# Kernel optimization log

Measured on AMD Instinct MI355X. Metric: run time of the kernel, lower is better.

Reference implementation:

```python
import jax, jax.numpy as jnp
import numpy as np

S = 2048          # sequence length (single prefill sequence)
HID = 4096        # hidden_size
NH, NKV, HD = 32, 8, 128   # q heads, kv heads, head_dim
THETA = 10000.0
SCALE = HD ** -0.5


def setup_inputs() -> dict:
    key = jax.random.key(0)
    k1, k2, k3 = jax.random.split(key, 3)
    hidden_states = jax.random.normal(k1, (S, HID), jnp.float32)
    positions = jnp.arange(S, dtype=jnp.int32)
    W_qkv = jax.random.normal(k2, (HID, (NH + 2 * NKV) * HD), jnp.float32) * 0.02
    W_o = jax.random.normal(k3, (NH * HD, HID), jnp.float32) * 0.02
    return {"hidden_states": hidden_states, "positions": positions,
            "W_qkv": W_qkv, "W_o": W_o}


def _rope(x, positions):
    # x: [T, H, HD]; neox-style RoPE (rotate halves, is_neox_style=True)
    half = HD // 2
    inv_freq = 1.0 / (THETA ** (jnp.arange(half, dtype=jnp.float32) / half))
    freqs = positions.astype(jnp.float32)[:, None] * inv_freq[None, :]  # [T, half]
    cos = jnp.cos(freqs)[:, None, :]
    sin = jnp.sin(freqs)[:, None, :]
    x1, x2 = x[..., :half], x[..., half:]
    return jnp.concatenate([x1 * cos - x2 * sin, x2 * cos + x1 * sin], axis=-1)


def reference(hidden_states, positions, W_qkv, W_o):
    # fused QKV projection then split (q_size = NH*HD, kv_size = NKV*HD)
    qkv = hidden_states @ W_qkv                      # [S, (NH+2*NKV)*HD]
    q, k, v = jnp.split(qkv, [NH * HD, NH * HD + NKV * HD], axis=1)
    q = _rope(q.reshape(S, NH, HD), positions)       # [S, NH, HD]
    k = _rope(k.reshape(S, NKV, HD), positions)      # [S, NKV, HD]
    v = v.reshape(S, NKV, HD)
    # GQA: broadcast kv heads to query heads
    rep = NH // NKV
    k = jnp.repeat(k, rep, axis=1)                   # [S, NH, HD]
    v = jnp.repeat(v, rep, axis=1)
    scores = jnp.einsum('qhd,khd->hqk', q, k) * SCALE  # [NH, S, S]
    causal = jnp.tril(jnp.ones((S, S), dtype=bool))
    scores = jnp.where(causal[None], scores, jnp.finfo(scores.dtype).min)
    attn = jax.nn.softmax(scores, axis=-1)
    out = jnp.einsum('hqk,khd->qhd', attn, v).reshape(S, NH * HD)
    return out @ W_o                                 # [S, HID]
```

## Files before the change

kernel.cpp:

```cpp
#include <hip/hip_runtime.h>
#include <math.h>
#include <stdint.h>

#define S_LEN 2048
#define HID 4096
#define NH 32
#define NKV 8
#define HD 128
#define QKV_N ((NH + 2*NKV) * HD)
#define NQK (NH + NKV)
static __device__ __constant__ const float SCALE_F = 0.08838834764831845f;

typedef __bf16 bf16x8 __attribute__((ext_vector_type(8)));
typedef __bf16 bf16x4 __attribute__((ext_vector_type(4)));
typedef float  f32x4  __attribute__((ext_vector_type(4)));
typedef uint32_t u32x4 __attribute__((ext_vector_type(4)));

#define GLD_LDS(gptr, lptr) \
  __builtin_amdgcn_global_load_lds( \
      (const __attribute__((address_space(1))) uint32_t*)(gptr), \
      (__attribute__((address_space(3))) uint32_t*)(lptr), 16, 0, 0)

__global__ void cast_bf16_kernel(const float4* __restrict__ in, __bf16* __restrict__ out, int n4) {
  int i = blockIdx.x * blockDim.x + threadIdx.x;
  if (i >= n4) return;
  float4 v = in[i];
  bf16x4 o = { (__bf16)v.x, (__bf16)v.y, (__bf16)v.z, (__bf16)v.w };
  *(bf16x4*)(out + (size_t)i * 4) = o;
}

__global__ void transpose_cast_kernel(const float* __restrict__ in, __bf16* __restrict__ out,
                                      int R, int C) {
  __shared__ float tile[32][33];
  int bx = blockIdx.x * 32;
  int by = blockIdx.y * 32;
  int tx = threadIdx.x, ty = threadIdx.y;
  for (int i = 0; i < 32; i += 8)
    tile[ty + i][tx] = in[(size_t)(by + ty + i) * C + bx + tx];
  __syncthreads();
  for (int i = 0; i < 32; i += 8)
    out[(size_t)(bx + ty + i) * R + by + tx] = (__bf16)tile[tx][ty + i];
}

__global__ void transpose_v_kernel(const __bf16* __restrict__ qkv, __bf16* __restrict__ Vt) {
  __shared__ __bf16 tile[32][33];
  int kvh = blockIdx.z;
  int sb = blockIdx.x * 32;
  int db = blockIdx.y * 32;
  int tx = threadIdx.x, ty = threadIdx.y;
  const __bf16* src = qkv + (size_t)(NH + NKV) * HD + (size_t)kvh * HD;
  for (int i = 0; i < 32; i += 8)
    tile[ty + i][tx] = src[(size_t)(sb + ty + i) * QKV_N + db + tx];
  __syncthreads();
  for (int i = 0; i < 32; i += 8)
    Vt[((size_t)kvh * HD + db + ty + i) * S_LEN + sb + tx] = tile[tx][ty + i];
}

__global__ void rope_kernel(const __bf16* __restrict__ qkv, const int* __restrict__ pos,
                            __bf16* __restrict__ Qr, __bf16* __restrict__ Kr) {
  int idx = blockIdx.x * blockDim.x + threadIdx.x;
  int half = idx & 63;
  int t = idx >> 6;
  int hh = t % NQK;
  int s = t / NQK;
  if (s >= S_LEN) return;
  float p = (float)pos[s];
  float inv_freq = exp2f((float)half * -0.2076205059304601f);
  float ang = p * inv_freq;
  float cs = cosf(ang), sn = sinf(ang);
  const __bf16* src; __bf16* dst;
  if (hh < NH) {
    src = qkv + (size_t)s * QKV_N + (size_t)hh * HD;
    dst = Qr + ((size_t)s * NH + hh) * HD;
  } else {
    int kh = hh - NH;
    src = qkv + (size_t)s * QKV_N + (size_t)NH * HD + (size_t)kh * HD;
    dst = Kr + ((size_t)s * NKV + kh) * HD;
  }
  float x1 = (float)src[half], x2 = (float)src[half + 64];
  dst[half]      = (__bf16)(x1 * cs - x2 * sn);
  dst[half + 64] = (__bf16)(x2 * cs + x1 * sn);
}

template <typename OutT>
__global__ __launch_bounds__(512, 2) void gemm8p_kernel(const __bf16* __restrict__ A,
                                                        const __bf16* __restrict__ Bt,
                                                        OutT* __restrict__ C,
                                                        int M, int N, int K) {
  __shared__ __align__(16) __bf16 sA[2][2][256 * 32];
  __shared__ __align__(16) __bf16 sB[2][2][256 * 32];
  const int tid = threadIdx.x;
  const int lane = tid & 63;
  const int wave = tid >> 6;
  const int quad = lane >> 4;
  const int l16 = lane & 15;
  const int wm = (wave >> 2) * 128;
  const int wn = (wave & 3) * 64;

  const int nx = gridDim.x;
  const int nwg = nx * gridDim.y;
  int bid = blockIdx.y * nx + blockIdx.x;
  int swz = (bid & 7) * (nwg >> 3) + (bid >> 3);
  const size_t bm = (size_t)(swz / nx) * 256;
  const size_t bn = (size_t)(swz % nx) * 256;

  const int NT = K >> 6;
  const int rsw = (l16 >> 1) & 3;

  f32x4 acc[8][4] = {};
  bf16x8 aR[4], bR[4];

  typedef __attribute__((address_space(3))) __bf16 lds_bf16;
  const uint32_t sAb = (uint32_t)(uintptr_t)(lds_bf16*)&sA[0][0][0];
  const uint32_t sBb = (uint32_t)(uintptr_t)(lds_bf16*)&sB[0][0][0];
  const uint32_t aBase = sAb + (uint32_t)(((wm + l16) * 32 + (quad ^ rsw) * 8) * 2);
  const uint32_t bBase = sBb + (uint32_t)(((wn + l16) * 32 + (quad ^ rsw) * 8) * 2);

#define DSRD4(dst, baseaddr) do {                                                 \
    u32x4 t0_, t1_, t2_, t3_;                                                     \
    asm volatile("ds_read_b128 %0, %4\n\t"                                        \
                 "ds_read_b128 %1, %4 offset:1024\n\t"                            \
                 "ds_read_b128 %2, %4 offset:2048\n\t"                            \
                 "ds_read_b128 %3, %4 offset:3072"                                \
                 : "=&v"(t0_), "=&v"(t1_), "=&v"(t2_), "=&v"(t3_)                 \
                 : "v"(baseaddr));                                                \
    dst[0] = __builtin_bit_cast(bf16x8, t0_);                                     \
    dst[1] = __builtin_bit_cast(bf16x8, t1_);                                     \
    dst[2] = __builtin_bit_cast(bf16x8, t2_);                                     \
    dst[3] = __builtin_bit_cast(bf16x8, t3_);                                     \
  } while (0)

#define LOADB(bf, kk) DSRD4(bR, bBase + (bf) * 32768u + (kk) * 16384u)
#define LOADA(bf, kk, ih) DSRD4(aR, aBase + (bf) * 32768u + (kk) * 16384u + (ih) * 4096u)

#define STAGE(gbase, rowbase, tau, h, dst) do {                                   \
    size_t kof_ = (size_t)((tau) % NT) * 64 + (h) * 32;                           \
    _Pragma("unroll")                                                             \
    for (int it_ = 0; it_ < 2; ++it_) {                                           \
      int c_ = it_ * 512 + tid;                                                   \
      int row_ = c_ >> 2, ch_ = c_ & 3;                                           \
      int chL_ = ch_ ^ ((row_ >> 1) & 3);                                         \
      GLD_LDS(&(gbase)[((rowbase) + row_) * (size_t)K + kof_ + chL_ * 8],         \
              &(dst)[c_ * 8]);                                                    \
    }                                                                             \
  } while (0)

#define MFMA16(ih) do {                                                           \
    __builtin_amdgcn_s_setprio(1);                                                \
    _Pragma("unroll")                                                             \
    for (int i_ = 0; i_ < 4; ++i_)                                                \
      _Pragma("unroll")                                                           \
      for (int j_ = 0; j_ < 4; ++j_)                                              \
        acc[(ih) * 4 + i_][j_] = __builtin_amdgcn_mfma_f32_16x16x32_bf16(         \
            aR[i_], bR[j_], acc[(ih) * 4 + i_][j_], 0, 0, 0);                     \
    __builtin_amdgcn_s_setprio(0);                                                \
    __builtin_amdgcn_sched_barrier(0);                                            \
  } while (0)

#define BAR() __builtin_amdgcn_s_barrier()
#define LGKM0() do { asm volatile("s_waitcnt lgkmcnt(0)");                        \
                     __builtin_amdgcn_sched_barrier(0); } while (0)
#define VMCNT4() asm volatile("s_waitcnt vmcnt(4)" ::: "memory")

  STAGE(A,  bm, 0, 0, sA[0][0]);
  STAGE(Bt, bn, 0, 0, sB[0][0]);
  STAGE(A,  bm, 0, 1, sA[0][1]);
  STAGE(Bt, bn, 0, 1, sB[0][1]);
  STAGE(A,  bm, 1, 0, sA[1][0]);
  STAGE(Bt, bn, 1, 0, sB[1][0]);
  VMCNT4();
  BAR();

  for (int u = 0; u < (NT >> 1); ++u) {
    const int t0 = 2 * u;
    LOADB(0, 0); LOADA(0, 0, 0);
    STAGE(A, bm, t0 + 1, 1, sA[1][1]);
    BAR();
    LGKM0();
    MFMA16(0);
    BAR();
    LOADA(0, 0, 1);
    STAGE(Bt, bn, t0 + 1, 1, sB[1][1]);
    BAR();
    LGKM0();
    MFMA16(1);
    BAR();
    LOADB(0, 1); LOADA(0, 1, 0);
    STAGE(A, bm, t0 + 2, 0, sA[0][0]);
    BAR();
    LGKM0();
    MFMA16(0);
    BAR();
    LOADA(0, 1, 1);
    STAGE(Bt, bn, t0 + 2, 0, sB[0][0]);
    BAR();
    LGKM0();
    MFMA16(1);
    VMCNT4();
    BAR();
    LOADB(1, 0); LOADA(1, 0, 0);
    STAGE(A, bm, t0 + 2, 1, sA[0][1]);
    BAR();
    LGKM0();
    MFMA16(0);
    BAR();
    LOADA(1, 0, 1);
    STAGE(Bt, bn, t0 + 2, 1, sB[0][1]);
    BAR();
    LGKM0();
    MFMA16(1);
    BAR();
    LOADB(1, 1); LOADA(1, 1, 0);
    STAGE(A, bm, t0 + 3, 0, sA[1][0]);
    BAR();
    LGKM0();
    MFMA16(0);
    BAR();
    LOADA(1, 1, 1);
    STAGE(Bt, bn, t0 + 3, 0, sB[1][0]);
    BAR();
    LGKM0();
    MFMA16(1);
    VMCNT4();
    BAR();
  }

  asm volatile("s_waitcnt vmcnt(0)" ::: "memory");

  #pragma unroll
  for (int i = 0; i < 8; ++i)
    #pragma unroll
    for (int j = 0; j < 4; ++j)
      #pragma unroll
      for (int r = 0; r < 4; ++r) {
        size_t row = bm + wm + i * 16 + quad * 4 + r;
        size_t col = bn + wn + j * 16 + l16;
        C[row * (size_t)N + col] = (OutT)acc[i][j][r];
      }

#undef STAGE
#undef LOADB
#undef LOADA
#undef DSRD4
#undef MFMA16
#undef BAR
#undef LGKM0
#undef VMCNT4
}

__global__ __launch_bounds__(256, 2) void attn_kernel(const __bf16* __restrict__ Qr,
                                                      const __bf16* __restrict__ Kr,
                                                      const __bf16* __restrict__ Vt,
                                                      __bf16* __restrict__ O) {
  __shared__ __align__(16) char smem[73728];
  __bf16* Ps = (__bf16*)(smem + 65536);

  const int bid = blockIdx.x;
  const int h = bid & (NH - 1);
  const int qb = (S_LEN / 64 - 1) - (bid >> 5);
  const int kvh = h >> 2;
  const int tid = threadIdx.x;
  const int lane = tid & 63, wave = tid >> 6;
  const int quad = lane >> 4, l16 = lane & 15;
  const int sw = l16 & 7;
  const int q0 = qb * 64;

#define STAGE_KV(kbase, bufv) do {                                                 \
    char* kd_ = smem + (bufv) * 16384;                                             \
    char* vd_ = smem + 32768 + (bufv) * 16384;                                     \
    _Pragma("unroll")                                                              \
    for (int pass_ = 0; pass_ < 4; ++pass_) {                                      \
      int c_ = pass_ * 256 + tid;                                                  \
      int row_ = c_ >> 4, ch_ = c_ & 15;                                           \
      int chs_ = ch_ ^ (row_ & 7);                                                 \
      GLD_LDS(&Kr[(size_t)((kbase) + row_) * (NKV * HD) + (size_t)kvh * HD + chs_ * 8], \
              kd_ + c_ * 16);                                                      \
    }                                                                              \
    _Pragma("unroll")                                                              \
    for (int pass_ = 0; pass_ < 4; ++pass_) {                                      \
      int c_ = pass_ * 256 + tid;                                                  \
      int d_ = c_ >> 3, ch_ = c_ & 7;                                              \
      int chs_ = ch_ ^ (d_ & 7);                                                   \
      GLD_LDS(&Vt[((size_t)kvh * HD + d_) * S_LEN + (kbase) + chs_ * 8],           \
              vd_ + c_ * 16);                                                      \
    }                                                                              \
  } while (0)

  bf16x8 qf[4];
  {
    const __bf16* qp = Qr + (size_t)(q0 + wave * 16 + l16) * (NH * HD) + (size_t)h * HD + quad * 8;
    for (int kk = 0; kk < 4; ++kk) qf[kk] = *(const bf16x8*)(qp + kk * 32);
  }
  f32x4 oacc[8] = {};
  float m2 = -INFINITY, l_i = 0.0f;
  const float C2 = SCALE_F * 1.4426950408889634f;

  int buf = 0;
  STAGE_KV(0, 0);
  for (int kb = 0; kb <= q0; kb += 64) {
    __syncthreads();
    if (kb + 64 <= q0) STAGE_KV(kb + 64, buf ^ 1);

    const __bf16* Ks = (const __bf16*)(smem + buf * 16384);
    const __bf16* Vs = (const __bf16*)(smem + 32768 + buf * 16384);

    f32x4 sc[4] = {};
    __builtin_amdgcn_s_setprio(1);
    for (int jt = 0; jt < 4; ++jt)
      for (int kk = 0; kk < 4; ++kk) {
        bf16x8 kf = *(const bf16x8*)&Ks[(jt * 16 + l16) * 128 + ((kk * 4 + quad) ^ sw) * 8];
        sc[jt] = __builtin_amdgcn_mfma_f32_16x16x32_bf16(kf, qf[kk], sc[jt], 0, 0, 0);
      }
    __builtin_amdgcn_s_setprio(0);

    float s[16];
    for (int jt = 0; jt < 4; ++jt)
      for (int r = 0; r < 4; ++r) s[jt * 4 + r] = sc[jt][r];
    if (kb == q0) {
      int qloc = wave * 16 + l16;
      for (int jt = 0; jt < 4; ++jt)
        for (int r = 0; r < 4; ++r)
          if (jt * 16 + quad * 4 + r > qloc) s[jt * 4 + r] = -INFINITY;
    }
    float mx = s[0];
    for (int i = 1; i < 16; ++i) mx = fmaxf(mx, s[i]);
    mx = fmaxf(mx, __shfl_xor(mx, 16, 64));
    mx = fmaxf(mx, __shfl_xor(mx, 32, 64));
    float m2new = fmaxf(m2, mx * C2);
    float alpha = exp2f(m2 - m2new);
    float pv[16], sum = 0.0f;
    for (int i = 0; i < 16; ++i) { pv[i] = exp2f(fmaf(s[i], C2, -m2new)); sum += pv[i]; }
    sum += __shfl_xor(sum, 16, 64);
    sum += __shfl_xor(sum, 32, 64);
    l_i = l_i * alpha + sum;
    m2 = m2new;
    for (int dt = 0; dt < 8; ++dt) oacc[dt] *= alpha;

    __bf16* pw = Ps + wave * 1024 + l16 * 64;
    for (int jt = 0; jt < 4; ++jt) {
      bf16x4 pk = { (__bf16)pv[jt*4+0], (__bf16)pv[jt*4+1], (__bf16)pv[jt*4+2], (__bf16)pv[jt*4+3] };
      int chunk = jt * 2 + (quad >> 1);
      *(bf16x4*)&pw[((chunk ^ sw) * 8) + (quad & 1) * 4] = pk;
    }
    __builtin_amdgcn_s_setprio(1);
    for (int half = 0; half < 2; ++half) {
      bf16x8 pf = *(const bf16x8*)&pw[((half * 4 + quad) ^ sw) * 8];
      for (int dt = 0; dt < 8; ++dt) {
        bf16x8 vf = *(const bf16x8*)&Vs[(dt * 16 + l16) * 64 + ((half * 4 + quad) ^ sw) * 8];
        oacc[dt] = __builtin_amdgcn_mfma_f32_16x16x32_bf16(vf, pf, oacc[dt], 0, 0, 0);
      }
    }
    __builtin_amdgcn_s_setprio(0);
    buf ^= 1;
  }
  __syncthreads();

#undef STAGE_KV

  float* scr = (float*)smem + wave * 2112;
  float inv = 1.0f / l_i;
  for (int dt = 0; dt < 8; ++dt) {
    f32x4 v = oacc[dt] * inv;
    *(f32x4*)&scr[l16 * 132 + dt * 16 + quad * 4] = v;
  }
  for (int it = 0; it < 4; ++it) {
    int c = it * 64 + lane;
    int row = c >> 4, ch = c & 15;
    const float* sp = &scr[row * 132 + ch * 8];
    f32x4 a = *(const f32x4*)sp;
    f32x4 b = *(const f32x4*)(sp + 4);
    bf16x8 o = { (__bf16)a[0], (__bf16)a[1], (__bf16)a[2], (__bf16)a[3],
                 (__bf16)b[0], (__bf16)b[1], (__bf16)b[2], (__bf16)b[3] };
    *(bf16x8*)&O[(size_t)(q0 + wave * 16 + row) * (NH * HD) + (size_t)h * HD + ch * 8] = o;
  }
}

extern "C" void kernel_launch(void* const* d_in, const int* in_sizes, int n_in,
                              void* d_out, int out_size, void* d_ws, size_t ws_size,
                              hipStream_t stream) {
  const float* hidden    = (const float*)d_in[0];
  const int*   positions = (const int*)d_in[1];
  const float* Wqkv      = (const float*)d_in[2];
  const float* Wo        = (const float*)d_in[3];
  float* out = (float*)d_out;

  char* p = (char*)d_ws;
  auto alloc = [&](size_t bytes) { char* r = p; p += (bytes + 255) & ~(size_t)255; return r; };
  __bf16* hid_bf = (__bf16*)alloc((size_t)S_LEN * HID * 2);
  __bf16* wqkvT  = (__bf16*)alloc((size_t)QKV_N * HID * 2);
  __bf16* woT    = (__bf16*)alloc((size_t)HID * HID * 2);
  __bf16* qkv    = (__bf16*)alloc((size_t)S_LEN * QKV_N * 2);
  __bf16* Qr     = (__bf16*)alloc((size_t)S_LEN * NH * HD * 2);
  __bf16* Kr     = (__bf16*)alloc((size_t)S_LEN * NKV * HD * 2);
  __bf16* Vt     = (__bf16*)alloc((size_t)S_LEN * NKV * HD * 2);
  __bf16* attn   = hid_bf;

  {
    int n4 = S_LEN * HID / 4;
    cast_bf16_kernel<<<(n4 + 255) / 256, 256, 0, stream>>>((const float4*)hidden, hid_bf, n4);
  }
  transpose_cast_kernel<<<dim3(QKV_N / 32, HID / 32), dim3(32, 8), 0, stream>>>(Wqkv, wqkvT, HID, QKV_N);
  transpose_cast_kernel<<<dim3(HID / 32, HID / 32), dim3(32, 8), 0, stream>>>(Wo, woT, HID, HID);
  gemm8p_kernel<__bf16><<<dim3(QKV_N / 256, S_LEN / 256), 512, 0, stream>>>(
      hid_bf, wqkvT, qkv, S_LEN, QKV_N, HID);
  {
    int total = S_LEN * NQK * 64;
    rope_kernel<<<total / 256, 256, 0, stream>>>(qkv, positions, Qr, Kr);
  }
  transpose_v_kernel<<<dim3(S_LEN / 32, HD / 32, NKV), dim3(32, 8), 0, stream>>>(qkv, Vt);
  attn_kernel<<<NH * (S_LEN / 64), 256, 0, stream>>>(Qr, Kr, Vt, attn);
  gemm8p_kernel<float><<<dim3(HID / 256, S_LEN / 256), 512, 0, stream>>>(
      attn, woT, out, S_LEN, HID, HID);
}
```

Before: 539.7 us.

## Double-buffer LDS fragment registers and pipeline GEMM staging with inline asm

The 256x256 bf16 GEMM main loop is restructured. Fragment registers are double-buffered so the ds_reads for the next MFMA group are issued before the current group runs, with partial lgkmcnt waits replacing full drains. Global-to-LDS staging becomes inline asm that uses precomputed pointer increments and m0 set from a scalar. The block-to-tile mapping is also changed to an XCD-aware one. This should hide LDS latency and cut address arithmetic and barriers, at the cost of more VGPRs and fragile hand-counted wait values.

```diff
diff --git a/kernel.cpp b/kernel.cpp
--- a/kernel.cpp
+++ b/kernel.cpp
@@ -98,23 +98,46 @@
   const int wn = (wave & 3) * 64;
 
   const int nx = gridDim.x;
-  const int nwg = nx * gridDim.y;
-  int bid = blockIdx.y * nx + blockIdx.x;
-  int swz = (bid & 7) * (nwg >> 3) + (bid >> 3);
-  const size_t bm = (size_t)(swz / nx) * 256;
-  const size_t bn = (size_t)(swz % nx) * 256;
+  size_t bm, bn;
+  if (gridDim.y == 8 && (nx & 7) == 0) {
+    int lin = blockIdx.y * nx + blockIdx.x;
+    int j = lin >> 3, xcd = lin & 7;
+    bm = (size_t)(j & 7) * 256;
+    bn = (size_t)(xcd * (nx >> 3) + (j >> 3)) * 256;
+  } else {
+    bm = (size_t)blockIdx.y * 256;
+    bn = (size_t)blockIdx.x * 256;
+  }
 
   const int NT = K >> 6;
   const int rsw = (l16 >> 1) & 3;
 
   f32x4 acc[8][4] = {};
-  bf16x8 aR[4], bR[4];
+  bf16x8 aR[2][4], bR[2][4];
+
+  const int row0 = tid >> 2;
+  const int chL = (tid & 3) ^ ((tid >> 3) & 3);
+  const uint64_t off128 = (uint64_t)128 * K * 2;
+  uint64_t aGA = (uint64_t)(uintptr_t)A + ((bm + row0) * (size_t)K) * 2 + (size_t)chL * 16;
+  uint64_t bGA = (uint64_t)(uintptr_t)Bt + ((bn + row0) * (size_t)K) * 2 + (size_t)chL * 16;
 
   typedef __attribute__((address_space(3))) __bf16 lds_bf16;
   const uint32_t sAb = (uint32_t)(uintptr_t)(lds_bf16*)&sA[0][0][0];
   const uint32_t sBb = (uint32_t)(uintptr_t)(lds_bf16*)&sB[0][0][0];
+  const uint32_t wlds = (uint32_t)__builtin_amdgcn_readfirstlane(wave * 1024);
   const uint32_t aBase = sAb + (uint32_t)(((wm + l16) * 32 + (quad ^ rsw) * 8) * 2);
   const uint32_t bBase = sBb + (uint32_t)(((wn + l16) * 32 + (quad ^ rsw) * 8) * 2);
+
+#define LDSA(bf, kk) (sAb + (bf) * 32768u + (kk) * 16384u)
+#define LDSB(bf, kk) (sBb + (bf) * 32768u + (kk) * 16384u)
+
+#define STAGE_ASM(ga, ldsbase) \
+  asm volatile("s_mov_b32 m0, %0\n\t" \
+               "global_load_lds_dwordx4 %2, off\n\t" \
+               "s_mov_b32 m0, %1\n\t" \
+               "global_load_lds_dwordx4 %3, off" \
+               :: "s"((ldsbase) + wlds), "s"((ldsbase) + wlds + 8192u), \
+                  "v"(ga), "v"((ga) + off128) : "memory")
 
 #define DSRD4(dst, baseaddr) do {                                                 \
     u32x4 t0_, t1_, t2_, t3_;                                                     \
@@ -130,102 +153,90 @@
     dst[3] = __builtin_bit_cast(bf16x8, t3_);                                     \
   } while (0)
 
-#define LOADB(bf, kk) DSRD4(bR, bBase + (bf) * 32768u + (kk) * 16384u)
-#define LOADA(bf, kk, ih) DSRD4(aR, aBase + (bf) * 32768u + (kk) * 16384u + (ih) * 4096u)
-
-#define STAGE(gbase, rowbase, tau, h, dst) do {                                   \
-    size_t kof_ = (size_t)((tau) % NT) * 64 + (h) * 32;                           \
-    _Pragma("unroll")                                                             \
-    for (int it_ = 0; it_ < 2; ++it_) {                                           \
-      int c_ = it_ * 512 + tid;                                                   \
-      int row_ = c_ >> 2, ch_ = c_ & 3;                                           \
-      int chL_ = ch_ ^ ((row_ >> 1) & 3);                                         \
-      GLD_LDS(&(gbase)[((rowbase) + row_) * (size_t)K + kof_ + chL_ * 8],         \
-              &(dst)[c_ * 8]);                                                    \
-    }                                                                             \
-  } while (0)
-
-#define MFMA16(ih) do {                                                           \
+#define ISSUE_A(set, bf, kk, ih) DSRD4(aR[set], aBase + (bf) * 32768u + (kk) * 16384u + (ih) * 4096u)
+#define ISSUE_B(set, bf, kk)     DSRD4(bR[set], bBase + (bf) * 32768u + (kk) * 16384u)
+
+#define MFMA16(as, bs, ih) do {                                                   \
     __builtin_amdgcn_s_setprio(1);                                                \
     _Pragma("unroll")                                                             \
     for (int i_ = 0; i_ < 4; ++i_)                                                \
       _Pragma("unroll")                                                           \
       for (int j_ = 0; j_ < 4; ++j_)                                              \
         acc[(ih) * 4 + i_][j_] = __builtin_amdgcn_mfma_f32_16x16x32_bf16(         \
-            aR[i_], bR[j_], acc[(ih) * 4 + i_][j_], 0, 0, 0);                     \
+            aR[as][i_], bR[bs][j_], acc[(ih) * 4 + i_][j_], 0, 0, 0);             \
     __builtin_amdgcn_s_setprio(0);                                                \
     __builtin_amdgcn_sched_barrier(0);                                            \
   } while (0)
 
 #define BAR() __builtin_amdgcn_s_barrier()
-#define LGKM0() do { asm volatile("s_waitcnt lgkmcnt(0)");                        \
+#define LGKM4() do { asm volatile("s_waitcnt lgkmcnt(4)");                        \
                      __builtin_amdgcn_sched_barrier(0); } while (0)
-#define VMCNT4() asm volatile("s_waitcnt vmcnt(4)" ::: "memory")
-
-  STAGE(A,  bm, 0, 0, sA[0][0]);
-  STAGE(Bt, bn, 0, 0, sB[0][0]);
-  STAGE(A,  bm, 0, 1, sA[0][1]);
-  STAGE(Bt, bn, 0, 1, sB[0][1]);
-  STAGE(A,  bm, 1, 0, sA[1][0]);
-  STAGE(Bt, bn, 1, 0, sB[1][0]);
-  VMCNT4();
+#define LGKM8() do { asm volatile("s_waitcnt lgkmcnt(8)");                        \
+                     __builtin_amdgcn_sched_barrier(0); } while (0)
+#define VMCNT4() do { asm volatile("s_waitcnt vmcnt(4)");                         \
+                      __builtin_amdgcn_sched_barrier(0); } while (0)
+
+  STAGE_ASM(aGA,        LDSA(0, 0));
+  STAGE_ASM(bGA,        LDSB(0, 0));
+  STAGE_ASM(aGA + 64,   LDSA(0, 1));
+  STAGE_ASM(bGA + 64,   LDSB(0, 1));
+  STAGE_ASM(aGA + 128,  LDSA(1, 0));
+  STAGE_ASM(bGA + 128,  LDSB(1, 0));
+  aGA += 192; bGA += 192;
+  asm volatile("s_waitcnt vmcnt(8)");
+  __builtin_amdgcn_sched_barrier(0);
   BAR();
+  ISSUE_A(0, 0, 0, 0); ISSUE_B(0, 0, 0);
 
   for (int u = 0; u < (NT >> 1); ++u) {
-    const int t0 = 2 * u;
-    LOADB(0, 0); LOADA(0, 0, 0);
-    STAGE(A, bm, t0 + 1, 1, sA[1][1]);
-    BAR();
-    LGKM0();
-    MFMA16(0);
-    BAR();
-    LOADA(0, 0, 1);
-    STAGE(Bt, bn, t0 + 1, 1, sB[1][1]);
-    BAR();
-    LGKM0();
-    MFMA16(1);
-    BAR();
-    LOADB(0, 1); LOADA(0, 1, 0);
-    STAGE(A, bm, t0 + 2, 0, sA[0][0]);
-    BAR();
-    LGKM0();
-    MFMA16(0);
-    BAR();
-    LOADA(0, 1, 1);
-    STAGE(Bt, bn, t0 + 2, 0, sB[0][0]);
-    BAR();
-    LGKM0();
-    MFMA16(1);
     VMCNT4();
-    BAR();
-    LOADB(1, 0); LOADA(1, 0, 0);
-    STAGE(A, bm, t0 + 2, 1, sA[0][1]);
-    BAR();
-    LGKM0();
-    MFMA16(0);
-    BAR();
-    LOADA(1, 0, 1);
-    STAGE(Bt, bn, t0 + 2, 1, sB[0][1]);
-    BAR();
-    LGKM0();
-    MFMA16(1);
-    BAR();
-    LOADB(1, 1); LOADA(1, 1, 0);
-    STAGE(A, bm, t0 + 3, 0, sA[1][0]);
-    BAR();
-    LGKM0();
-    MFMA16(0);
-    BAR();
-    LOADA(1, 1, 1);
-    STAGE(Bt, bn, t0 + 3, 0, sB[1][0]);
-    BAR();
-    LGKM0();
-    MFMA16(1);
+    ISSUE_A(1, 0, 0, 1);
+    BAR();
+    LGKM4();
+    MFMA16(0, 0, 0);
+    STAGE_ASM(aGA, LDSA(1, 1)); aGA += 64;
+    ISSUE_A(0, 0, 1, 0); ISSUE_B(1, 0, 1);
+    BAR();
+    LGKM8();
+    MFMA16(1, 0, 1);
+    STAGE_ASM(bGA, LDSB(1, 1)); bGA += 64;
     VMCNT4();
-    BAR();
-  }
-
-  asm volatile("s_waitcnt vmcnt(0)" ::: "memory");
+    ISSUE_A(1, 0, 1, 1);
+    BAR();
+    LGKM4();
+    MFMA16(0, 1, 0);
+    STAGE_ASM(aGA, LDSA(0, 0)); aGA += 64;
+    ISSUE_A(0, 1, 0, 0); ISSUE_B(0, 1, 0);
+    BAR();
+    LGKM8();
+    MFMA16(1, 1, 1);
+    STAGE_ASM(bGA, LDSB(0, 0)); bGA += 64;
+    VMCNT4();
+    ISSUE_A(1, 1, 0, 1);
+    BAR();
+    LGKM4();
+    MFMA16(0, 0, 0);
+    STAGE_ASM(aGA, LDSA(0, 1)); aGA += 64;
+    ISSUE_A(0, 1, 1, 0); ISSUE_B(1, 1, 1);
+    BAR();
+    LGKM8();
+    MFMA16(1, 0, 1);
+    STAGE_ASM(bGA, LDSB(0, 1)); bGA += 64;
+    VMCNT4();
+    ISSUE_A(1, 1, 1, 1);
+    BAR();
+    LGKM4();
+    MFMA16(0, 1, 0);
+    STAGE_ASM(aGA, LDSA(1, 0)); aGA += 64;
+    ISSUE_A(0, 0, 0, 0); ISSUE_B(0, 0, 0);
+    BAR();
+    LGKM8();
+    MFMA16(1, 1, 1);
+    STAGE_ASM(bGA, LDSB(1, 0)); bGA += 64;
+  }
+
+  asm volatile("s_waitcnt vmcnt(0) lgkmcnt(0)");
+  __builtin_amdgcn_sched_barrier(0);
 
   #pragma unroll
   for (int i = 0; i < 8; ++i)
@@ -238,13 +249,16 @@
         C[row * (size_t)N + col] = (OutT)acc[i][j][r];
       }
 
-#undef STAGE
-#undef LOADB
-#undef LOADA
+#undef LDSA
+#undef LDSB
+#undef STAGE_ASM
 #undef DSRD4
+#undef ISSUE_A
+#undef ISSUE_B
 #undef MFMA16
 #undef BAR
-#undef LGKM0
+#undef LGKM4
+#undef LGKM8
 #undef VMCNT4
 }
 
```

Result: faster. 496.9 us (-7.9%).
